# Optimization experiments

Measured on AMD Instinct MI355X. Metric: run time of the kernel, lower is better.

## Reference

```python
import jax, jax.numpy as jnp
import numpy as np

B, DIM, HID = 16384, 512, 256
DT, N_STEPS = 0.1, 3


def setup_inputs() -> dict:
    key = jax.random.key(0)
    ks = jax.random.split(key, 5)
    z = jax.random.normal(ks[0], (B, DIM), dtype=jnp.float32)
    # HNN energy MLP: 2*DIM -> HID -> HID -> 1 (tanh activations)
    s1 = 1.0 / np.sqrt(2 * DIM)
    s2 = 1.0 / np.sqrt(HID)
    W1 = jax.random.normal(ks[1], (2 * DIM, HID), dtype=jnp.float32) * s1
    b1 = jnp.zeros((HID,), dtype=jnp.float32)
    W2 = jax.random.normal(ks[2], (HID, HID), dtype=jnp.float32) * s2
    b2 = jnp.zeros((HID,), dtype=jnp.float32)
    W3 = jax.random.normal(ks[3], (HID, 1), dtype=jnp.float32) * s2
    b3 = jnp.zeros((1,), dtype=jnp.float32)
    return {"z": z, "W1": W1, "b1": b1, "W2": W2, "b2": b2, "W3": W3, "b3": b3}


def reference(z, W1, b1, W2, b2, W3, b3):
    d = z.shape[-1]
    dt = jnp.float32(DT)

    def H_sum(zp):  # total Hamiltonian over the batch -> scalar
        h = jnp.tanh(zp @ W1 + b1)
        h = jnp.tanh(h @ W2 + b2)
        return jnp.sum(h @ W3 + b3)

    gradH = jax.grad(H_sum)  # [B, 2d]: (dH/dq, dH/dp) per sample

    def leapfrog(zp):
        q, p = zp[:, :d], zp[:, d:]
        # half-step momentum: dp/dt = -dH/dq
        g = gradH(jnp.concatenate([q, p], axis=-1))
        p = p - 0.5 * dt * g[:, :d]
        # full-step position: dq/dt = dH/dp
        g = gradH(jnp.concatenate([q, p], axis=-1))
        q = q + dt * g[:, d:]
        # half-step momentum
        g = gradH(jnp.concatenate([q, p], axis=-1))
        p = p - 0.5 * dt * g[:, :d]
        return jnp.concatenate([q, p], axis=-1)

    zp = jnp.concatenate([z, jnp.zeros_like(z)], axis=-1)  # phase space [B, 2d]
    for _ in range(N_STEPS):  # fixed small unroll (n_steps=3)
        zp = leapfrog(zp)
    return zp[:, :d]
```

## Files before the change

kernel.cpp:

```cpp
#include <hip/hip_runtime.h>
#include <math.h>

#define DT 0.1f

typedef __attribute__((ext_vector_type(4)))  short short4v;
typedef __attribute__((ext_vector_type(8)))  short short8;
typedef __attribute__((ext_vector_type(16))) float f32x16;

__device__ __forceinline__ short f2bf(float x) {
    unsigned int u = __float_as_uint(x);
    unsigned int r = (u + 0x7fffu + ((u >> 16) & 1u)) >> 16;
    return (short)r;
}
__device__ __forceinline__ float bf2f(short s) {
    return __uint_as_float(((unsigned int)(unsigned short)s) << 16);
}
__device__ __forceinline__ float tanh_fast(float x) {
    float e = __expf(x + x);
    float r = __builtin_amdgcn_rcpf(e + 1.f);
    return __builtin_fmaf(-2.f, r, 1.f);
}

__global__ __launch_bounds__(256)
void pack32_direct(const float* __restrict__ W, short* __restrict__ out, int K, int N)
{
    int idx = blockIdx.x * 256 + threadIdx.x;
    int j = idx & 7, lane = (idx >> 3) & 63, rest = idx >> 9;
    int KT = K >> 4;
    int kt = rest % KT, nt = rest / KT;
    int k = kt * 16 + (lane >> 5) * 8 + j;
    int n = nt * 32 + (lane & 31);
    out[idx] = f2bf(W[k * N + n]);
}
__global__ __launch_bounds__(256)
void pack32_trans(const float* __restrict__ W, short* __restrict__ out, int K, int N)
{
    int idx = blockIdx.x * 256 + threadIdx.x;
    int j = idx & 7, lane = (idx >> 3) & 63, rest = idx >> 9;
    int KT = K >> 4;
    int kt = rest % KT, nt = rest / KT;
    int k = kt * 16 + (lane >> 5) * 8 + j;
    int n = nt * 32 + (lane & 31);
    out[idx] = f2bf(W[n * K + k]);
}

__global__ __launch_bounds__(256)
void pack_zA(const float* __restrict__ z, short* __restrict__ out)
{
    __shared__ short zb[32 * 520];
    const int tid = threadIdx.x;
    const int bx = blockIdx.x;
#pragma unroll
    for (int j = 0; j < 16; ++j) {
        int lin = j * 256 + tid;
        int r = lin >> 7, c4 = lin & 127;
        float4 v = ((const float4*)z)[(size_t)(bx * 32 + r) * 128 + c4];
        short4v pk;
        pk.x = f2bf(v.x); pk.y = f2bf(v.y); pk.z = f2bf(v.z); pk.w = f2bf(v.w);
        *(short4v*)&zb[r * 520 + c4 * 4] = pk;
    }
    __syncthreads();
    const int lane = tid & 63, w = tid >> 6;
    const int m = lane & 31, lh = lane >> 5;
#pragma unroll
    for (int j = 0; j < 8; ++j) {
        int kt = w * 8 + j;
        short8 f = *(const short8*)&zb[m * 520 + kt * 16 + lh * 8];
        *(short8*)(out + (((size_t)bx * 32 + kt) * 64 + lane) * 8) = f;
    }
}

__global__ __launch_bounds__(256)
void compute_S(const float* __restrict__ W1, float* __restrict__ Sq, float* __restrict__ Sp)
{
    int n = threadIdx.x;
    int b = blockIdx.x;
    float s = 0.f;
    if (b < 256) {
        int k = b;
        for (int c = 0; c < 512; ++c)
            s = __builtin_fmaf(W1[c * 256 + k], W1[(512 + c) * 256 + n], s);
        Sq[k * 256 + n] = -0.5f * DT * s;
    } else {
        int k = b - 256;
        for (int c = 0; c < 512; ++c)
            s = __builtin_fmaf(W1[(512 + c) * 256 + k], W1[c * 256 + n], s);
        Sp[k * 256 + n] = DT * s;
    }
}

__device__ __forceinline__ short8 lds_frag(const short* Ac, int kt, int mt2,
                                           int l31, int lh, int rot)
{
    int nt_s = kt >> 1;
    int po = (((kt & 1) * 2 + lh) * 4 + rot) & 15;
    int base = ((nt_s * 2 + mt2) * 64 + l31) * 16 + po;
    short4v x = *(const short4v*)&Ac[base];
    short4v y = *(const short4v*)&Ac[base + 512];
    short8 r;
    r[0] = x.x; r[1] = x.y; r[2] = x.z; r[3] = x.w;
    r[4] = y.x; r[5] = y.y; r[6] = y.z; r[7] = y.w;
    return r;
}
__device__ __forceinline__ void store_tile(short* Ac, int nt, int mt2, int lane,
                                           int rot, const f32x16 v)
{
    int base = ((nt * 2 + mt2) * 64 + lane) * 16;
#pragma unroll
    for (int c = 0; c < 4; ++c) {
        short4v pk;
        pk.x = f2bf(v[4 * c + 0]); pk.y = f2bf(v[4 * c + 1]);
        pk.z = f2bf(v[4 * c + 2]); pk.w = f2bf(v[4 * c + 3]);
        *(short4v*)&Ac[base + ((4 * c + rot) & 15)] = pk;
    }
}

__device__ __forceinline__ void gemm_nt(const short* Ac, int l31, int lh, int rot,
                                        const short8* __restrict__ Bf,
                                        f32x16& acc0, f32x16& acc1)
{
    short8 pb[4];
#pragma unroll
    for (int k = 0; k < 4; ++k) pb[k] = Bf[k * 64];
    short8 pa0 = lds_frag(Ac, 0, 0, l31, lh, rot);
    short8 pa1 = lds_frag(Ac, 0, 1, l31, lh, rot);
#pragma unroll
    for (int kt = 0; kt < 16; ++kt) {
        short8 ca0 = pa0, ca1 = pa1, cb = pb[kt & 3];
        if (kt + 4 < 16) pb[kt & 3] = Bf[(kt + 4) * 64];
        if (kt + 1 < 16) {
            pa0 = lds_frag(Ac, kt + 1, 0, l31, lh, rot);
            pa1 = lds_frag(Ac, kt + 1, 1, l31, lh, rot);
        }
        acc0 = __builtin_amdgcn_mfma_f32_32x32x16_bf16(ca0, cb, acc0, 0, 0, 0);
        acc1 = __builtin_amdgcn_mfma_f32_32x32x16_bf16(ca1, cb, acc1, 0, 0, 0);
    }
}

__global__ __launch_bounds__(512, 2)
void mega(const short* __restrict__ zpA,
          const short* __restrict__ PB1q,
          const short* __restrict__ PB2,
          const short* __restrict__ PB2T,
          const short* __restrict__ PBSq,
          const short* __restrict__ PBSp,
          const float* __restrict__ b1,
          const float* __restrict__ b2,
          const float* __restrict__ W3,
          short* __restrict__ dsumP)
{
    __shared__ short h1_c[16384];
    __shared__ short da_c[16384];

    const int tid = threadIdx.x;
    const int lane = tid & 63, w = tid >> 6;
    const int l31 = lane & 31, lh = lane >> 5;
    const int rot = ((l31 >> 2) & 3) * 4;
    const int bx = blockIdx.x;

    const int col = w * 32 + l31;
    const float b1v = b1[col], b2v = b2[col], w3v = W3[col];

    f32x16 A1[2];  A1[0] = 0.f; A1[1] = 0.f;
    f32x16 dsum[2]; dsum[0] = 0.f; dsum[1] = 0.f;

    {
        const short8* Af0 = (const short8*)zpA + ((size_t)(bx * 2 + 0) * 32) * 64 + lane;
        const short8* Af1 = (const short8*)zpA + ((size_t)(bx * 2 + 1) * 32) * 64 + lane;
        const short8* Bf  = (const short8*)PB1q + ((size_t)w * 32) * 64 + lane;
        short8 pa0[2], pa1[2], pb[4];
#pragma unroll
        for (int k = 0; k < 2; ++k) { pa0[k] = Af0[k * 64]; pa1[k] = Af1[k * 64]; }
#pragma unroll
        for (int k = 0; k < 4; ++k) pb[k] = Bf[k * 64];
#pragma unroll
        for (int kt = 0; kt < 32; ++kt) {
            short8 ca0 = pa0[kt & 1], ca1 = pa1[kt & 1], cb = pb[kt & 3];
            if (kt + 2 < 32) {
                pa0[kt & 1] = Af0[(kt + 2) * 64];
                pa1[kt & 1] = Af1[(kt + 2) * 64];
            }
            if (kt + 4 < 32) pb[kt & 3] = Bf[(kt + 4) * 64];
            A1[0] = __builtin_amdgcn_mfma_f32_32x32x16_bf16(ca0, cb, A1[0], 0, 0, 0);
            A1[1] = __builtin_amdgcn_mfma_f32_32x32x16_bf16(ca1, cb, A1[1], 0, 0, 0);
        }
    }

    for (int it = 0; it < 8; ++it) {
        const bool isq = ((it % 3) == 1);

#pragma unroll
        for (int t = 0; t < 2; ++t) {
            f32x16 hv;
#pragma unroll
            for (int r = 0; r < 16; ++r) hv[r] = tanh_fast(A1[t][r] + b1v);
            store_tile(h1_c, w, t, lane, rot, hv);
        }
        __syncthreads();

        {
            f32x16 t0 = 0.f, t1 = 0.f;
            gemm_nt(h1_c, l31, lh, rot, (const short8*)PB2 + ((size_t)w * 16) * 64 + lane, t0, t1);
#pragma unroll
            for (int t = 0; t < 2; ++t) {
                f32x16& tt = t ? t1 : t0;
                f32x16 d;
#pragma unroll
                for (int r = 0; r < 16; ++r) {
                    float ta = tanh_fast(tt[r] + b2v);
                    d[r] = w3v * (1.f - ta * ta);
                }
                store_tile(da_c, w, t, lane, rot, d);
            }
        }
        __syncthreads();

        {
            f32x16 t0 = 0.f, t1 = 0.f;
            gemm_nt(da_c, l31, lh, rot, (const short8*)PB2T + ((size_t)w * 16) * 64 + lane, t0, t1);
            __syncthreads();
#pragma unroll
            for (int t = 0; t < 2; ++t) {
                f32x16& tt = t ? t1 : t0;
                f32x16 d;
                const int basei = ((w * 2 + t) * 64 + lane) * 16;
#pragma unroll
                for (int c = 0; c < 4; ++c) {
                    short4v h4 = *(const short4v*)&h1_c[basei + ((4 * c + rot) & 15)];
                    float h0 = bf2f(h4.x), h1f = bf2f(h4.y);
                    float h2 = bf2f(h4.z), h3 = bf2f(h4.w);
                    d[4 * c + 0] = tt[4 * c + 0] * (1.f - h0 * h0);
                    d[4 * c + 1] = tt[4 * c + 1] * (1.f - h1f * h1f);
                    d[4 * c + 2] = tt[4 * c + 2] * (1.f - h2 * h2);
                    d[4 * c + 3] = tt[4 * c + 3] * (1.f - h3 * h3);
                }
                if (isq) dsum[t] += d;
                store_tile(da_c, w, t, lane, rot, d);
            }
        }
        __syncthreads();

        if (it < 7) {
            const short* S = isq ? PBSp : PBSq;
            gemm_nt(da_c, l31, lh, rot, (const short8*)S + ((size_t)w * 16) * 64 + lane,
                    A1[0], A1[1]);
        }
    }

    store_tile(da_c, w, 0, lane, rot, dsum[0]);
    store_tile(da_c, w, 1, lane, rot, dsum[1]);
    __syncthreads();
    const int mt2 = w >> 2;
#pragma unroll
    for (int kk = 0; kk < 4; ++kk) {
        int kt = (w & 3) * 4 + kk;
        short8 f = lds_frag(da_c, kt, mt2, l31, lh, rot);
        *(short8*)(dsumP + (((size_t)(bx * 2 + mt2) * 16 + kt) * 64 + lane) * 8) = f;
    }
}

__global__ __launch_bounds__(512, 2)
void out_gemm(const short* __restrict__ dsumP, const short* __restrict__ PB1Tp,
              const float* __restrict__ z, float* __restrict__ out)
{
    __shared__ float Ct[32 * 512];

    const int tid = threadIdx.x;
    const int lane = tid & 63, w = tid >> 6;
    const int mt2 = w >> 2, nq = w & 3;
    const int l31 = lane & 31, lh = lane >> 5;
    const int bx = blockIdx.x;
    const int rt32 = bx * 2 + mt2;

    f32x16 acc[4];
#pragma unroll
    for (int t = 0; t < 4; ++t) acc[t] = 0.f;

    const short8* Af = (const short8*)dsumP + (size_t)rt32 * 16 * 64 + lane;
    const short8* Bf[4];
#pragma unroll
    for (int t = 0; t < 4; ++t)
        Bf[t] = (const short8*)PB1Tp + (size_t)(nq * 4 + t) * 16 * 64 + lane;

    short8 ar[2], br[2][4];
#pragma unroll
    for (int k = 0; k < 2; ++k) {
        ar[k] = Af[k * 64];
#pragma unroll
        for (int t = 0; t < 4; ++t) br[k][t] = Bf[t][k * 64];
    }
#pragma unroll
    for (int kt = 0; kt < 16; ++kt) {
        short8 a = ar[kt & 1];
        short8 bb[4];
#pragma unroll
        for (int t = 0; t < 4; ++t) bb[t] = br[kt & 1][t];
        if (kt + 2 < 16) {
            ar[kt & 1] = Af[(kt + 2) * 64];
#pragma unroll
            for (int t = 0; t < 4; ++t) br[kt & 1][t] = Bf[t][(kt + 2) * 64];
        }
#pragma unroll
        for (int t = 0; t < 4; ++t)
            acc[t] = __builtin_amdgcn_mfma_f32_32x32x16_bf16(a, bb[t], acc[t], 0, 0, 0);
    }

#pragma unroll
    for (int p = 0; p < 2; ++p) {
        if (mt2 == p) {
#pragma unroll
            for (int t = 0; t < 4; ++t) {
                const int c = (nq * 4 + t) * 32 + l31;
#pragma unroll
                for (int r = 0; r < 16; ++r) {
                    int row = (r & 3) + 8 * (r >> 2) + 4 * lh;
                    Ct[row * 512 + c] = acc[t][r];
                }
            }
        }
        __syncthreads();
#pragma unroll
        for (int j = 0; j < 8; ++j) {
            int lin = j * 512 + tid;
            int r = lin >> 7, c4 = lin & 127;
            size_t gi = (size_t)(bx * 64 + p * 32 + r) * 128 + c4;
            float4 zv = ((const float4*)z)[gi];
            float4 cv = *(const float4*)&Ct[r * 512 + c4 * 4];
            float4 ov;
            ov.x = zv.x + DT * cv.x; ov.y = zv.y + DT * cv.y;
            ov.z = zv.z + DT * cv.z; ov.w = zv.w + DT * cv.w;
            ((float4*)out)[gi] = ov;
        }
        __syncthreads();
    }
}

extern "C" void kernel_launch(void* const* d_in, const int* in_sizes, int n_in,
                              void* d_out, int out_size, void* d_ws, size_t ws_size,
                              hipStream_t stream)
{
    const float* z  = (const float*)d_in[0];
    const float* W1 = (const float*)d_in[1];
    const float* b1 = (const float*)d_in[2];
    const float* W2 = (const float*)d_in[3];
    const float* b2 = (const float*)d_in[4];
    const float* W3 = (const float*)d_in[5];
    float* out = (float*)d_out;

    float* Sq_f  = (float*)d_ws;
    float* Sp_f  = Sq_f + 65536;
    short* PB2   = (short*)(Sp_f + 65536);
    short* PB2T  = PB2   + 65536;
    short* PBSq  = PB2T  + 65536;
    short* PBSp  = PBSq  + 65536;
    short* PB1q  = PBSp  + 65536;
    short* PB1Tp = PB1q  + 131072;
    short* zpA   = PB1Tp + 131072;
    short* dsumP = zpA   + 8388608;

    compute_S<<<512, 256, 0, stream>>>(W1, Sq_f, Sp_f);
    pack32_direct<<<256, 256, 0, stream>>>(W2, PB2, 256, 256);
    pack32_trans <<<256, 256, 0, stream>>>(W2, PB2T, 256, 256);
    pack32_direct<<<256, 256, 0, stream>>>(Sq_f, PBSq, 256, 256);
    pack32_direct<<<256, 256, 0, stream>>>(Sp_f, PBSp, 256, 256);
    pack32_direct<<<512, 256, 0, stream>>>(W1, PB1q, 512, 256);
    pack32_trans <<<512, 256, 0, stream>>>(W1 + 512 * 256, PB1Tp, 256, 512);
    pack_zA<<<512, 256, 0, stream>>>(z, zpA);

    mega<<<256, 512, 0, stream>>>(zpA, PB1q, PB2, PB2T, PBSq, PBSp,
                                  b1, b2, W3, dsumP);
    out_gemm<<<256, 512, 0, stream>>>(dsumP, PB1Tp, z, out);
}
```

Measured before the change: 216.8 us.

## Fuse z packing and output GEMM into mega kernel with 16 waves

Folds the z bf16 packing and the final dsum×W1pᵀ output GEMM into the main kernel, so the zpA and dsumP intermediates never round-trip through global memory. The mega kernel now uses 1024 threads with one 32x32 tile per wave instead of two, for more waves per block. It also merges the weight-packing kernels and computes S directly in packed bf16, which cuts the launch count from ten to three. In exchange, the output GEMM now runs inside the register-heavy kernel, per-wave MFMA reuse is lower, and the output stores are narrower scalar writes.

```diff
diff --git a/kernel.cpp b/kernel.cpp
--- a/kernel.cpp
+++ b/kernel.cpp
@@ -21,72 +21,67 @@
     return __builtin_fmaf(-2.f, r, 1.f);
 }
 
+__device__ __forceinline__ int bfrag_idx(int k, int n, int KT) {
+    int nt = n >> 5, l31 = n & 31;
+    int kt = k >> 4, lh = (k >> 3) & 1, j = k & 7;
+    return (((nt * KT + kt) * 64) + lh * 32 + l31) * 8 + j;
+}
+
 __global__ __launch_bounds__(256)
-void pack32_direct(const float* __restrict__ W, short* __restrict__ out, int K, int N)
-{
-    int idx = blockIdx.x * 256 + threadIdx.x;
-    int j = idx & 7, lane = (idx >> 3) & 63, rest = idx >> 9;
-    int KT = K >> 4;
-    int kt = rest % KT, nt = rest / KT;
-    int k = kt * 16 + (lane >> 5) * 8 + j;
-    int n = nt * 32 + (lane & 31);
-    out[idx] = f2bf(W[k * N + n]);
-}
+void packW(const float* __restrict__ W1, const float* __restrict__ W2,
+           short* __restrict__ PB2, short* __restrict__ PB2T,
+           short* __restrict__ PB1q, short* __restrict__ PB1Tp)
+{
+    int bx = blockIdx.x, tid = threadIdx.x;
+    if (bx < 256) {
+        int idx = bx * 256 + tid;
+        int j = idx & 7, lane = (idx >> 3) & 63, rest = idx >> 9;
+        int kt = rest % 16, nt = rest / 16;
+        int k = kt * 16 + (lane >> 5) * 8 + j, n = nt * 32 + (lane & 31);
+        PB2[idx] = f2bf(W2[k * 256 + n]);
+    } else if (bx < 512) {
+        int idx = (bx - 256) * 256 + tid;
+        int j = idx & 7, lane = (idx >> 3) & 63, rest = idx >> 9;
+        int kt = rest % 16, nt = rest / 16;
+        int k = kt * 16 + (lane >> 5) * 8 + j, n = nt * 32 + (lane & 31);
+        PB2T[idx] = f2bf(W2[n * 256 + k]);
+    } else if (bx < 1024) {
+        int idx = (bx - 512) * 256 + tid;
+        int j = idx & 7, lane = (idx >> 3) & 63, rest = idx >> 9;
+        int kt = rest % 32, nt = rest / 32;
+        int k = kt * 16 + (lane >> 5) * 8 + j, n = nt * 32 + (lane & 31);
+        PB1q[idx] = f2bf(W1[k * 256 + n]);
+    } else {
+        int idx = (bx - 1024) * 256 + tid;
+        int j = idx & 7, lane = (idx >> 3) & 63, rest = idx >> 9;
+        int kt = rest % 16, nt = rest / 16;
+        int k = kt * 16 + (lane >> 5) * 8 + j, n = nt * 32 + (lane & 31);
+        PB1Tp[idx] = f2bf(W1[(512 + n) * 256 + k]);
+    }
+}
+
 __global__ __launch_bounds__(256)
-void pack32_trans(const float* __restrict__ W, short* __restrict__ out, int K, int N)
-{
-    int idx = blockIdx.x * 256 + threadIdx.x;
-    int j = idx & 7, lane = (idx >> 3) & 63, rest = idx >> 9;
-    int KT = K >> 4;
-    int kt = rest % KT, nt = rest / KT;
-    int k = kt * 16 + (lane >> 5) * 8 + j;
-    int n = nt * 32 + (lane & 31);
-    out[idx] = f2bf(W[n * K + k]);
-}
-
-__global__ __launch_bounds__(256)
-void pack_zA(const float* __restrict__ z, short* __restrict__ out)
-{
-    __shared__ short zb[32 * 520];
-    const int tid = threadIdx.x;
+void compute_S_packed(const float* __restrict__ W1,
+                      short* __restrict__ PBSq, short* __restrict__ PBSp)
+{
+    const int n = threadIdx.x;
     const int bx = blockIdx.x;
-#pragma unroll
-    for (int j = 0; j < 16; ++j) {
-        int lin = j * 256 + tid;
-        int r = lin >> 7, c4 = lin & 127;
-        float4 v = ((const float4*)z)[(size_t)(bx * 32 + r) * 128 + c4];
-        short4v pk;
-        pk.x = f2bf(v.x); pk.y = f2bf(v.y); pk.z = f2bf(v.z); pk.w = f2bf(v.w);
-        *(short4v*)&zb[r * 520 + c4 * 4] = pk;
-    }
-    __syncthreads();
-    const int lane = tid & 63, w = tid >> 6;
-    const int m = lane & 31, lh = lane >> 5;
-#pragma unroll
-    for (int j = 0; j < 8; ++j) {
-        int kt = w * 8 + j;
-        short8 f = *(const short8*)&zb[m * 520 + kt * 16 + lh * 8];
-        *(short8*)(out + (((size_t)bx * 32 + kt) * 64 + lane) * 8) = f;
-    }
-}
-
-__global__ __launch_bounds__(256)
-void compute_S(const float* __restrict__ W1, float* __restrict__ Sq, float* __restrict__ Sp)
-{
-    int n = threadIdx.x;
-    int b = blockIdx.x;
-    float s = 0.f;
-    if (b < 256) {
-        int k = b;
-        for (int c = 0; c < 512; ++c)
-            s = __builtin_fmaf(W1[c * 256 + k], W1[(512 + c) * 256 + n], s);
-        Sq[k * 256 + n] = -0.5f * DT * s;
-    } else {
-        int k = b - 256;
-        for (int c = 0; c < 512; ++c)
-            s = __builtin_fmaf(W1[(512 + c) * 256 + k], W1[c * 256 + n], s);
-        Sp[k * 256 + n] = DT * s;
-    }
+    const bool isp = bx >= 32;
+    const int k0 = (isp ? bx - 32 : bx) * 8;
+    float s[8] = {0.f, 0.f, 0.f, 0.f, 0.f, 0.f, 0.f, 0.f};
+    const float* Wn = W1 + (isp ? 0 : 512 * 256);
+    const float* Wk = W1 + (isp ? 512 * 256 : 0);
+    for (int c = 0; c < 512; ++c) {
+        float wn = Wn[c * 256 + n];
+#pragma unroll
+        for (int i = 0; i < 8; ++i)
+            s[i] = __builtin_fmaf(Wk[c * 256 + k0 + i], wn, s[i]);
+    }
+    const float coef = isp ? DT : -0.5f * DT;
+    short* dst = isp ? PBSp : PBSq;
+#pragma unroll
+    for (int i = 0; i < 8; ++i)
+        dst[bfrag_idx(k0 + i, n, 16)] = f2bf(coef * s[i]);
 }
 
 __device__ __forceinline__ short8 lds_frag(const short* Ac, int kt, int mt2,
@@ -115,223 +110,160 @@
     }
 }
 
-__device__ __forceinline__ void gemm_nt(const short* Ac, int l31, int lh, int rot,
-                                        const short8* __restrict__ Bf,
-                                        f32x16& acc0, f32x16& acc1)
+__device__ __forceinline__ void gemm_nt1(const short* Ac, int mt, int l31, int lh,
+                                         int rot, const short8* __restrict__ Bf,
+                                         f32x16& acc)
 {
     short8 pb[4];
 #pragma unroll
     for (int k = 0; k < 4; ++k) pb[k] = Bf[k * 64];
-    short8 pa0 = lds_frag(Ac, 0, 0, l31, lh, rot);
-    short8 pa1 = lds_frag(Ac, 0, 1, l31, lh, rot);
+    short8 pa = lds_frag(Ac, 0, mt, l31, lh, rot);
 #pragma unroll
     for (int kt = 0; kt < 16; ++kt) {
-        short8 ca0 = pa0, ca1 = pa1, cb = pb[kt & 3];
+        short8 ca = pa, cb = pb[kt & 3];
         if (kt + 4 < 16) pb[kt & 3] = Bf[(kt + 4) * 64];
-        if (kt + 1 < 16) {
-            pa0 = lds_frag(Ac, kt + 1, 0, l31, lh, rot);
-            pa1 = lds_frag(Ac, kt + 1, 1, l31, lh, rot);
-        }
-        acc0 = __builtin_amdgcn_mfma_f32_32x32x16_bf16(ca0, cb, acc0, 0, 0, 0);
-        acc1 = __builtin_amdgcn_mfma_f32_32x32x16_bf16(ca1, cb, acc1, 0, 0, 0);
-    }
-}
-
-__global__ __launch_bounds__(512, 2)
-void mega(const short* __restrict__ zpA,
+        if (kt + 1 < 16) pa = lds_frag(Ac, kt + 1, mt, l31, lh, rot);
+        acc = __builtin_amdgcn_mfma_f32_32x32x16_bf16(ca, cb, acc, 0, 0, 0);
+    }
+}
+
+__global__ __launch_bounds__(1024, 4)
+void mega(const float* __restrict__ z,
           const short* __restrict__ PB1q,
           const short* __restrict__ PB2,
           const short* __restrict__ PB2T,
           const short* __restrict__ PBSq,
           const short* __restrict__ PBSp,
+          const short* __restrict__ PB1Tp,
           const float* __restrict__ b1,
           const float* __restrict__ b2,
           const float* __restrict__ W3,
-          short* __restrict__ dsumP)
-{
-    __shared__ short h1_c[16384];
-    __shared__ short da_c[16384];
+          float* __restrict__ out)
+{
+    __shared__ short smem[32768];
+    short* const h1_c = smem;
+    short* const da_c = smem + 16384;
 
     const int tid = threadIdx.x;
     const int lane = tid & 63, w = tid >> 6;
+    const int nt = w & 7, mt = w >> 3;
     const int l31 = lane & 31, lh = lane >> 5;
     const int rot = ((l31 >> 2) & 3) * 4;
     const int bx = blockIdx.x;
 
-    const int col = w * 32 + l31;
+    const int col = nt * 32 + l31;
     const float b1v = b1[col], b2v = b2[col], w3v = W3[col];
 
-    f32x16 A1[2];  A1[0] = 0.f; A1[1] = 0.f;
-    f32x16 dsum[2]; dsum[0] = 0.f; dsum[1] = 0.f;
+    f32x16 A1 = 0.f, dsum = 0.f;
 
     {
-        const short8* Af0 = (const short8*)zpA + ((size_t)(bx * 2 + 0) * 32) * 64 + lane;
-        const short8* Af1 = (const short8*)zpA + ((size_t)(bx * 2 + 1) * 32) * 64 + lane;
-        const short8* Bf  = (const short8*)PB1q + ((size_t)w * 32) * 64 + lane;
-        short8 pa0[2], pa1[2], pb[4];
-#pragma unroll
-        for (int k = 0; k < 2; ++k) { pa0[k] = Af0[k * 64]; pa1[k] = Af1[k * 64]; }
-#pragma unroll
-        for (int k = 0; k < 4; ++k) pb[k] = Bf[k * 64];
-#pragma unroll
-        for (int kt = 0; kt < 32; ++kt) {
-            short8 ca0 = pa0[kt & 1], ca1 = pa1[kt & 1], cb = pb[kt & 3];
-            if (kt + 2 < 32) {
-                pa0[kt & 1] = Af0[(kt + 2) * 64];
-                pa1[kt & 1] = Af1[(kt + 2) * 64];
-            }
-            if (kt + 4 < 32) pb[kt & 3] = Bf[(kt + 4) * 64];
-            A1[0] = __builtin_amdgcn_mfma_f32_32x32x16_bf16(ca0, cb, A1[0], 0, 0, 0);
-            A1[1] = __builtin_amdgcn_mfma_f32_32x32x16_bf16(ca1, cb, A1[1], 0, 0, 0);
-        }
-    }
+        const short8* Bf = (const short8*)PB1q + ((size_t)nt * 32) * 64 + lane;
+        const int m = mt * 32 + l31;
+#pragma unroll
+        for (int c = 0; c < 2; ++c) {
+#pragma unroll
+            for (int j = 0; j < 4; ++j) {
+                int lin = j * 1024 + tid;
+                int r = lin >> 6, c4 = lin & 63;
+                float4 v = ((const float4*)z)[(size_t)(bx * 64 + r) * 128 + c * 64 + c4];
+                short4v pk;
+                pk.x = f2bf(v.x); pk.y = f2bf(v.y); pk.z = f2bf(v.z); pk.w = f2bf(v.w);
+                int unit = (c4 >> 1) ^ (r & 31);
+                *(short4v*)&smem[r * 256 + unit * 8 + (c4 & 1) * 4] = pk;
+            }
+            __syncthreads();
+            short8 pb[4];
+#pragma unroll
+            for (int k = 0; k < 4; ++k) pb[k] = Bf[(c * 16 + k) * 64];
+            short8 pa = *(const short8*)&smem[m * 256 + ((0 ^ (m & 31)) * 8)];
+#pragma unroll
+            for (int kt = 0; kt < 16; ++kt) {
+                short8 ca = pa, cb = pb[kt & 3];
+                if (kt + 4 < 16) pb[kt & 3] = Bf[(c * 16 + kt + 4) * 64];
+                if (kt + 1 < 16) {
+                    int unit = ((kt + 1) * 2 + lh) ^ (m & 31);
+                    pa = *(const short8*)&smem[m * 256 + unit * 8];
+                }
+                A1 = __builtin_amdgcn_mfma_f32_32x32x16_bf16(ca, cb, A1, 0, 0, 0);
+            }
+            __syncthreads();
+        }
+    }
+
+    const short8* PB2f  = (const short8*)PB2  + ((size_t)nt * 16) * 64 + lane;
+    const short8* PB2Tf = (const short8*)PB2T + ((size_t)nt * 16) * 64 + lane;
+    const short8* PBSqf = (const short8*)PBSq + ((size_t)nt * 16) * 64 + lane;
+    const short8* PBSpf = (const short8*)PBSp + ((size_t)nt * 16) * 64 + lane;
 
     for (int it = 0; it < 8; ++it) {
         const bool isq = ((it % 3) == 1);
 
-#pragma unroll
-        for (int t = 0; t < 2; ++t) {
+        {
             f32x16 hv;
 #pragma unroll
-            for (int r = 0; r < 16; ++r) hv[r] = tanh_fast(A1[t][r] + b1v);
-            store_tile(h1_c, w, t, lane, rot, hv);
+            for (int r = 0; r < 16; ++r) hv[r] = tanh_fast(A1[r] + b1v);
+            store_tile(h1_c, nt, mt, lane, rot, hv);
         }
         __syncthreads();
 
         {
-            f32x16 t0 = 0.f, t1 = 0.f;
-            gemm_nt(h1_c, l31, lh, rot, (const short8*)PB2 + ((size_t)w * 16) * 64 + lane, t0, t1);
-#pragma unroll
-            for (int t = 0; t < 2; ++t) {
-                f32x16& tt = t ? t1 : t0;
-                f32x16 d;
-#pragma unroll
-                for (int r = 0; r < 16; ++r) {
-                    float ta = tanh_fast(tt[r] + b2v);
-                    d[r] = w3v * (1.f - ta * ta);
-                }
-                store_tile(da_c, w, t, lane, rot, d);
-            }
+            f32x16 t0 = 0.f;
+            gemm_nt1(h1_c, mt, l31, lh, rot, PB2f, t0);
+            f32x16 d;
+#pragma unroll
+            for (int r = 0; r < 16; ++r) {
+                float ta = tanh_fast(t0[r] + b2v);
+                d[r] = w3v * (1.f - ta * ta);
+            }
+            store_tile(da_c, nt, mt, lane, rot, d);
         }
         __syncthreads();
 
         {
-            f32x16 t0 = 0.f, t1 = 0.f;
-            gemm_nt(da_c, l31, lh, rot, (const short8*)PB2T + ((size_t)w * 16) * 64 + lane, t0, t1);
+            f32x16 t0 = 0.f;
+            gemm_nt1(da_c, mt, l31, lh, rot, PB2Tf, t0);
+            float hv[16];
+            const int basei = ((nt * 2 + mt) * 64 + lane) * 16;
+#pragma unroll
+            for (int c = 0; c < 4; ++c) {
+                short4v h4 = *(const short4v*)&h1_c[basei + ((4 * c + rot) & 15)];
+                hv[4 * c + 0] = bf2f(h4.x); hv[4 * c + 1] = bf2f(h4.y);
+                hv[4 * c + 2] = bf2f(h4.z); hv[4 * c + 3] = bf2f(h4.w);
+            }
             __syncthreads();
-#pragma unroll
-            for (int t = 0; t < 2; ++t) {
-                f32x16& tt = t ? t1 : t0;
-                f32x16 d;
-                const int basei = ((w * 2 + t) * 64 + lane) * 16;
-#pragma unroll
-                for (int c = 0; c < 4; ++c) {
-                    short4v h4 = *(const short4v*)&h1_c[basei + ((4 * c + rot) & 15)];
-                    float h0 = bf2f(h4.x), h1f = bf2f(h4.y);
-                    float h2 = bf2f(h4.z), h3 = bf2f(h4.w);
-                    d[4 * c + 0] = tt[4 * c + 0] * (1.f - h0 * h0);
-                    d[4 * c + 1] = tt[4 * c + 1] * (1.f - h1f * h1f);
-                    d[4 * c + 2] = tt[4 * c + 2] * (1.f - h2 * h2);
-                    d[4 * c + 3] = tt[4 * c + 3] * (1.f - h3 * h3);
-                }
-                if (isq) dsum[t] += d;
-                store_tile(da_c, w, t, lane, rot, d);
-            }
+            f32x16 d;
+#pragma unroll
+            for (int r = 0; r < 16; ++r)
+                d[r] = t0[r] * (1.f - hv[r] * hv[r]);
+            if (isq) dsum += d;
+            store_tile(da_c, nt, mt, lane, rot, d);
         }
         __syncthreads();
 
         if (it < 7) {
-            const short* S = isq ? PBSp : PBSq;
-            gemm_nt(da_c, l31, lh, rot, (const short8*)S + ((size_t)w * 16) * 64 + lane,
-                    A1[0], A1[1]);
-        }
-    }
-
-    store_tile(da_c, w, 0, lane, rot, dsum[0]);
-    store_tile(da_c, w, 1, lane, rot, dsum[1]);
+            gemm_nt1(da_c, mt, l31, lh, rot, isq ? PBSpf : PBSqf, A1);
+        }
+    }
+
+    store_tile(da_c, nt, mt, lane, rot, dsum);
     __syncthreads();
-    const int mt2 = w >> 2;
-#pragma unroll
-    for (int kk = 0; kk < 4; ++kk) {
-        int kt = (w & 3) * 4 + kk;
-        short8 f = lds_frag(da_c, kt, mt2, l31, lh, rot);
-        *(short8*)(dsumP + (((size_t)(bx * 2 + mt2) * 16 + kt) * 64 + lane) * 8) = f;
-    }
-}
-
-__global__ __launch_bounds__(512, 2)
-void out_gemm(const short* __restrict__ dsumP, const short* __restrict__ PB1Tp,
-              const float* __restrict__ z, float* __restrict__ out)
-{
-    __shared__ float Ct[32 * 512];
-
-    const int tid = threadIdx.x;
-    const int lane = tid & 63, w = tid >> 6;
-    const int mt2 = w >> 2, nq = w & 3;
-    const int l31 = lane & 31, lh = lane >> 5;
-    const int bx = blockIdx.x;
-    const int rt32 = bx * 2 + mt2;
-
-    f32x16 acc[4];
-#pragma unroll
-    for (int t = 0; t < 4; ++t) acc[t] = 0.f;
-
-    const short8* Af = (const short8*)dsumP + (size_t)rt32 * 16 * 64 + lane;
-    const short8* Bf[4];
-#pragma unroll
-    for (int t = 0; t < 4; ++t)
-        Bf[t] = (const short8*)PB1Tp + (size_t)(nq * 4 + t) * 16 * 64 + lane;
-
-    short8 ar[2], br[2][4];
-#pragma unroll
-    for (int k = 0; k < 2; ++k) {
-        ar[k] = Af[k * 64];
-#pragma unroll
-        for (int t = 0; t < 4; ++t) br[k][t] = Bf[t][k * 64];
-    }
-#pragma unroll
-    for (int kt = 0; kt < 16; ++kt) {
-        short8 a = ar[kt & 1];
-        short8 bb[4];
-#pragma unroll
-        for (int t = 0; t < 4; ++t) bb[t] = br[kt & 1][t];
-        if (kt + 2 < 16) {
-            ar[kt & 1] = Af[(kt + 2) * 64];
-#pragma unroll
-            for (int t = 0; t < 4; ++t) br[kt & 1][t] = Bf[t][(kt + 2) * 64];
-        }
-#pragma unroll
-        for (int t = 0; t < 4; ++t)
-            acc[t] = __builtin_amdgcn_mfma_f32_32x32x16_bf16(a, bb[t], acc[t], 0, 0, 0);
-    }
-
-#pragma unroll
-    for (int p = 0; p < 2; ++p) {
-        if (mt2 == p) {
-#pragma unroll
-            for (int t = 0; t < 4; ++t) {
-                const int c = (nq * 4 + t) * 32 + l31;
-#pragma unroll
-                for (int r = 0; r < 16; ++r) {
-                    int row = (r & 3) + 8 * (r >> 2) + 4 * lh;
-                    Ct[row * 512 + c] = acc[t][r];
-                }
-            }
-        }
-        __syncthreads();
-#pragma unroll
-        for (int j = 0; j < 8; ++j) {
-            int lin = j * 512 + tid;
-            int r = lin >> 7, c4 = lin & 127;
-            size_t gi = (size_t)(bx * 64 + p * 32 + r) * 128 + c4;
-            float4 zv = ((const float4*)z)[gi];
-            float4 cv = *(const float4*)&Ct[r * 512 + c4 * 4];
-            float4 ov;
-            ov.x = zv.x + DT * cv.x; ov.y = zv.y + DT * cv.y;
-            ov.z = zv.z + DT * cv.z; ov.w = zv.w + DT * cv.w;
-            ((float4*)out)[gi] = ov;
-        }
-        __syncthreads();
+    {
+        const short8* Bo = (const short8*)PB1Tp + ((size_t)w * 16) * 64 + lane;
+        f32x16 oc[2];
+#pragma unroll
+        for (int m2 = 0; m2 < 2; ++m2) {
+            oc[m2] = 0.f;
+            gemm_nt1(da_c, m2, l31, lh, rot, Bo, oc[m2]);
+        }
+#pragma unroll
+        for (int m2 = 0; m2 < 2; ++m2) {
+#pragma unroll
+            for (int r = 0; r < 16; ++r) {
+                int row = bx * 64 + m2 * 32 + (r & 3) + 8 * (r >> 2) + 4 * lh;
+                size_t gi = (size_t)row * 512 + w * 32 + l31;
+                out[gi] = z[gi] + DT * oc[m2][r];
+            }
+        }
     }
 }
 
@@ -347,27 +279,15 @@
     const float* W3 = (const float*)d_in[5];
     float* out = (float*)d_out;
 
-    float* Sq_f  = (float*)d_ws;
-    float* Sp_f  = Sq_f + 65536;
-    short* PB2   = (short*)(Sp_f + 65536);
+    short* PBSq  = (short*)d_ws;
+    short* PBSp  = PBSq  + 65536;
+    short* PB2   = PBSp  + 65536;
     short* PB2T  = PB2   + 65536;
-    short* PBSq  = PB2T  + 65536;
-    short* PBSp  = PBSq  + 65536;
-    short* PB1q  = PBSp  + 65536;
+    short* PB1q  = PB2T  + 65536;
     short* PB1Tp = PB1q  + 131072;
-    short* zpA   = PB1Tp + 131072;
-    short* dsumP = zpA   + 8388608;
-
-    compute_S<<<512, 256, 0, stream>>>(W1, Sq_f, Sp_f);
-    pack32_direct<<<256, 256, 0, stream>>>(W2, PB2, 256, 256);
-    pack32_trans <<<256, 256, 0, stream>>>(W2, PB2T, 256, 256);
-    pack32_direct<<<256, 256, 0, stream>>>(Sq_f, PBSq, 256, 256);
-    pack32_direct<<<256, 256, 0, stream>>>(Sp_f, PBSp, 256, 256);
-    pack32_direct<<<512, 256, 0, stream>>>(W1, PB1q, 512, 256);
-    pack32_trans <<<512, 256, 0, stream>>>(W1 + 512 * 256, PB1Tp, 256, 512);
-    pack_zA<<<512, 256, 0, stream>>>(z, zpA);
-
-    mega<<<256, 512, 0, stream>>>(zpA, PB1q, PB2, PB2T, PBSq, PBSp,
-                                  b1, b2, W3, dsumP);
-    out_gemm<<<256, 512, 0, stream>>>(dsumP, PB1Tp, z, out);
-}
+
+    compute_S_packed<<<64, 256, 0, stream>>>(W1, PBSq, PBSp);
+    packW<<<1536, 256, 0, stream>>>(W1, W2, PB2, PB2T, PB1q, PB1Tp);
+    mega<<<256, 1024, 0, stream>>>(z, PB1q, PB2, PB2T, PBSq, PBSp, PB1Tp,
+                                   b1, b2, W3, out);
+}
```

After: 310.6 us. 43.3% more time.
